# Kernel optimization log

Measured on AMD Instinct MI355X. Metric: run time of the kernel, lower is better.

The kernel has to match this reference:

```python
import jax, jax.numpy as jnp
import numpy as np

N_NODES = 50000
N_EDGES = 1600000
D = 64  # in_dim = hidden_dim = out_dim
R = 8   # num_rels


def setup_inputs() -> dict:
    key = jax.random.key(0)
    ks = jax.random.split(key, 9)
    adj = jax.random.randint(ks[0], (2, N_EDGES), 0, N_NODES, dtype=jnp.int32)
    features = jax.random.normal(ks[1], (N_NODES, D), dtype=jnp.float32)
    edge_type = jax.random.randint(ks[2], (N_EDGES,), 0, R, dtype=jnp.int32)
    s = 1.0 / np.sqrt(D)
    W1 = jax.random.normal(ks[3], (R, D, D), dtype=jnp.float32) * s
    root1 = jax.random.normal(ks[4], (D, D), dtype=jnp.float32) * s
    b1 = jnp.zeros((D,), dtype=jnp.float32)
    W2 = jax.random.normal(ks[5], (R, D, D), dtype=jnp.float32) * s
    root2 = jax.random.normal(ks[6], (D, D), dtype=jnp.float32) * s
    b2 = jnp.zeros((D,), dtype=jnp.float32)
    return {"adj": adj, "features": features, "edge_type": edge_type,
            "W1": W1, "root1": root1, "b1": b1,
            "W2": W2, "root2": root2, "b2": b2}


def _rgcn_layer(x, edge_index, edge_type, W, root, bias):
    # FastRGCNConv, aggr='add': out_i = sum_{(j,r)->i} W_r x_j + root^T x_i + b
    src, dst = edge_index[0], edge_index[1]
    # pre-transform all nodes under every relation: [R, N, F]
    h = jnp.einsum('nd,rdf->rnf', x, W)
    msg = h[edge_type, src]                      # [E, F] gather per edge
    agg = jax.ops.segment_sum(msg, dst, num_segments=x.shape[0])
    return agg + x @ root + bias


def reference(adj, features, edge_type, W1, root1, b1, W2, root2, b2):
    x = _rgcn_layer(features, adj, edge_type, W1, root1, b1)
    x = jax.nn.relu(x)
    x = _rgcn_layer(x, adj, edge_type, W2, root2, b2)
    return x
```

## Files before the change

### kernel.cpp

```cpp
#include <hip/hip_runtime.h>
#include <cstdint>
#include <cstddef>

#define DF 64
#define NREL 8
#define DPB 64
#define DPB_SHIFT 6
#define NBMAX 1024
#define EPB 4096
#define BCAP 3072
#define NKEY 512

typedef __attribute__((ext_vector_type(8))) short bf16x8;
typedef __attribute__((ext_vector_type(4))) float f32x4;

static __device__ __forceinline__ unsigned short f2bf(float f) {
  unsigned int u = __float_as_uint(f);
  u += 0x7FFFu + ((u >> 16) & 1u);
  return (unsigned short)(u >> 16);
}
static __device__ __forceinline__ float bf2f(unsigned short s) {
  return __uint_as_float((unsigned int)s << 16);
}

__global__ __launch_bounds__(256) void to_bf16(
    const float* __restrict__ x, unsigned short* __restrict__ xb, int n8)
{
  int i = blockIdx.x * 256 + threadIdx.x;
  if (i >= n8) return;
  const float4 v0 = *(const float4*)&x[(size_t)i * 8];
  const float4 v1 = *(const float4*)&x[(size_t)i * 8 + 4];
  uint4 pk;
  pk.x = (unsigned)f2bf(v0.x) | ((unsigned)f2bf(v0.y) << 16);
  pk.y = (unsigned)f2bf(v0.z) | ((unsigned)f2bf(v0.w) << 16);
  pk.z = (unsigned)f2bf(v1.x) | ((unsigned)f2bf(v1.y) << 16);
  pk.w = (unsigned)f2bf(v1.z) | ((unsigned)f2bf(v1.w) << 16);
  *(uint4*)&xb[(size_t)i * 8] = pk;
}

__global__ __launch_bounds__(512) void pack_wfrag(
    const float* __restrict__ W1, const float* __restrict__ rt1,
    const float* __restrict__ W2, const float* __restrict__ rt2,
    bf16x8* __restrict__ frag)
{
  const int mat = blockIdx.x;
  const float* W = (mat < 8)  ? (W1 + (size_t)mat * 4096)
                 : (mat == 8) ? rt1
                 : (mat < 17) ? (W2 + (size_t)(mat - 9) * 4096)
                              : rt2;
  const int idx = threadIdx.x;
  const int ft = idx >> 7;
  const int ks = (idx >> 6) & 1;
  const int l  = idx & 63;
  const int col = ft * 16 + (l & 15);
  const int k0  = ks * 32 + (l >> 4) * 8;
  bf16x8 f;
#pragma unroll
  for (int j = 0; j < 8; ++j)
    f[j] = (short)f2bf(W[(size_t)(k0 + j) * 64 + col]);
  frag[(((size_t)mat * 4 + ft) * 2 + ks) * 64 + l] = f;
}

__global__ __launch_bounds__(256) void zero_ints(int* __restrict__ p, int n)
{
  int i = blockIdx.x * 256 + threadIdx.x;
  if (i < n) p[i] = 0;
}

__global__ __launch_bounds__(512) void bucket_count(
    const int* __restrict__ dst, int* __restrict__ bcnt,
    int* __restrict__ relof, int E, int NB)
{
  __shared__ int lh[NBMAX];
  const int t = threadIdx.x;
  for (int i = t; i < NB; i += 512) lh[i] = 0;
  __syncthreads();
  const int base = blockIdx.x * EPB;
  const int cnt = min(EPB, E - base);
  for (int k = t; k < cnt; k += 512)
    atomicAdd(&lh[dst[base + k] >> DPB_SHIFT], 1);
  __syncthreads();
  int* rrow = relof + (size_t)blockIdx.x * NB;
  for (int i = t; i < NB; i += 512) {
    int c = lh[i];
    rrow[i] = c ? atomicAdd(&bcnt[i], c) : 0;
  }
}

__global__ __launch_bounds__(1024) void scan_buckets(
    const int* __restrict__ bcnt, int* __restrict__ boff, int NB, int E)
{
  __shared__ int sc[1024];
  const int t = threadIdx.x;
  int v = (t < NB) ? bcnt[t] : 0;
  sc[t] = v;
  __syncthreads();
  for (int off = 1; off < 1024; off <<= 1) {
    int u = (t >= off) ? sc[t - off] : 0;
    __syncthreads();
    sc[t] += u;
    __syncthreads();
  }
  if (t < NB) boff[t] = sc[t] - v;
  if (t == 0) boff[NB] = E;
}

__global__ __launch_bounds__(512) void bin_scatter(
    const int* __restrict__ src, const int* __restrict__ dst,
    const int* __restrict__ et,
    const int* __restrict__ boff, const int* __restrict__ relof,
    unsigned int* __restrict__ binned, int E, int NB)
{
  __shared__ int cur[NBMAX];
  const int t = threadIdx.x;
  const int* rrow = relof + (size_t)blockIdx.x * NB;
  for (int i = t; i < NB; i += 512) cur[i] = boff[i] + rrow[i];
  __syncthreads();
  const int base = blockIdx.x * EPB;
  const int cnt = min(EPB, E - base);
  for (int k = t; k < cnt; k += 512) {
    int e = base + k;
    int d = dst[e];
    int pos = atomicAdd(&cur[d >> DPB_SHIFT], 1);
    binned[pos] = ((unsigned)et[e] << 24) | ((unsigned)src[e] << 7) |
                  ((unsigned)d & (DPB - 1));
  }
}

static __device__ __forceinline__ void gadd(
    float* __restrict__ acc, const uint4& u)
{
  acc[0] += bf2f((unsigned short)u.x);
  acc[1] += bf2f((unsigned short)(u.x >> 16));
  acc[2] += bf2f((unsigned short)u.y);
  acc[3] += bf2f((unsigned short)(u.y >> 16));
  acc[4] += bf2f((unsigned short)u.z);
  acc[5] += bf2f((unsigned short)(u.z >> 16));
  acc[6] += bf2f((unsigned short)u.w);
  acc[7] += bf2f((unsigned short)(u.w >> 16));
}

__global__ __launch_bounds__(512) void gather_sum(
    const unsigned int* __restrict__ binned,
    const int* __restrict__ boff,
    const unsigned short* __restrict__ xb,
    unsigned short* __restrict__ s,
    int N)
{
  __shared__ unsigned int srt[BCAP];
  __shared__ int h[NKEY], sc[NKEY], cur[NKEY];
  const int t = threadIdx.x;
  const int b = blockIdx.x;
  const int beg = boff[b], end = boff[b + 1];
  const int m = min(end - beg, BCAP);

  h[t] = 0;
  __syncthreads();
  for (int k = t; k < m; k += 512) {
    unsigned w = binned[beg + k];
    atomicAdd(&h[((w & (DPB - 1)) << 3) | (w >> 24)], 1);
  }
  __syncthreads();
  sc[t] = h[t];
  __syncthreads();
  for (int off = 1; off < NKEY; off <<= 1) {
    int u = (t >= off) ? sc[t - off] : 0;
    __syncthreads();
    sc[t] += u;
    __syncthreads();
  }
  cur[t] = sc[t] - h[t];
  __syncthreads();
  for (int k = t; k < m; k += 512) {
    unsigned w = binned[beg + k];
    int pos = atomicAdd(&cur[((w & (DPB - 1)) << 3) | (w >> 24)], 1);
    srt[pos] = w;
  }
  __syncthreads();

  const int nl = t >> 3;
  const int node = (b << DPB_SHIFT) + nl;
  const int l8 = (t & 7) * 8;
  if (node >= N) return;
  const int ovf = end - beg - BCAP;

#define XADDR(wv) ((const uint4*)&xb[(((size_t)(((wv) >> 7) & 0x1FFFFu)) << 6) + l8])
  for (int r = 0; r < NREL; ++r) {
    const int kk = (nl << 3) | r;
    int p = sc[kk] - h[kk];
    const int pe = sc[kk];
    float acc[8];
#pragma unroll
    for (int i = 0; i < 8; ++i) acc[i] = 0.f;

    for (; p + 3 < pe; p += 4) {
      unsigned w0 = srt[p],     w1 = srt[p + 1];
      unsigned w2 = srt[p + 2], w3 = srt[p + 3];
      uint4 u0 = *XADDR(w0), u1 = *XADDR(w1);
      uint4 u2 = *XADDR(w2), u3 = *XADDR(w3);
      gadd(acc, u0); gadd(acc, u1); gadd(acc, u2); gadd(acc, u3);
    }
    for (; p < pe; ++p) {
      unsigned w0 = srt[p];
      uint4 u0 = *XADDR(w0);
      gadd(acc, u0);
    }
    if (ovf > 0) {
      for (int k = 0; k < ovf; ++k) {
        unsigned w0 = binned[beg + BCAP + k];
        if ((int)(w0 & (DPB - 1)) == nl && (int)(w0 >> 24) == r) {
          uint4 u0 = *XADDR(w0);
          gadd(acc, u0);
        }
      }
    }

    uint4 pk;
    pk.x = (unsigned)f2bf(acc[0]) | ((unsigned)f2bf(acc[1]) << 16);
    pk.y = (unsigned)f2bf(acc[2]) | ((unsigned)f2bf(acc[3]) << 16);
    pk.z = (unsigned)f2bf(acc[4]) | ((unsigned)f2bf(acc[5]) << 16);
    pk.w = (unsigned)f2bf(acc[6]) | ((unsigned)f2bf(acc[7]) << 16);
    *(uint4*)&s[(((size_t)node * NREL + r) << 6) + l8] = pk;
  }
#undef XADDR
}

__global__ __launch_bounds__(256) void gemm_fused(
    const unsigned short* __restrict__ s,
    const unsigned short* __restrict__ xb,
    const bf16x8* __restrict__ wfrag,
    const float* __restrict__ bias,
    float* __restrict__ out,
    unsigned short* __restrict__ xbn,
    int N, int do_relu)
{
  const int tid = threadIdx.x;
  const int l  = tid & 63;
  const int w  = tid >> 6;
  const int n0 = blockIdx.x * 128 + w * 32;
  const int lr = l & 15;
  const int lg = l >> 4;

  f32x4 acc[4][2];
#pragma unroll
  for (int mt = 0; mt < 4; ++mt)
#pragma unroll
    for (int nt = 0; nt < 2; ++nt)
      acc[mt][nt] = (f32x4)(0.f);

  const int node0 = n0 + lr;
  const int node1 = n0 + 16 + lr;

  for (int r = 0; r < 9; ++r) {
    const bf16x8* wf = wfrag + (size_t)r * 512;
    bf16x8 a[4][2];
#pragma unroll
    for (int mt = 0; mt < 4; ++mt)
#pragma unroll
      for (int ks = 0; ks < 2; ++ks)
        a[mt][ks] = wf[(mt * 2 + ks) * 64 + l];

    bf16x8 b[2][2];
#pragma unroll
    for (int nt = 0; nt < 2; ++nt) {
      const int node = nt ? node1 : node0;
#pragma unroll
      for (int ks = 0; ks < 2; ++ks) {
        if (node < N) {
          const unsigned short* bp = (r < 8)
              ? &s[(((size_t)node * NREL + r) << 6) + ks * 32 + lg * 8]
              : &xb[((size_t)node << 6) + ks * 32 + lg * 8];
          b[nt][ks] = *(const bf16x8*)bp;
        } else {
          b[nt][ks] = (bf16x8)(short)0;
        }
      }
    }

#pragma unroll
    for (int ks = 0; ks < 2; ++ks)
#pragma unroll
      for (int mt = 0; mt < 4; ++mt)
#pragma unroll
        for (int nt = 0; nt < 2; ++nt)
          acc[mt][nt] = __builtin_amdgcn_mfma_f32_16x16x32_bf16(
              a[mt][ks], b[nt][ks], acc[mt][nt], 0, 0, 0);
  }

#pragma unroll
  for (int nt = 0; nt < 2; ++nt) {
    const int node = nt ? node1 : node0;
    if (node < N) {
#pragma unroll
      for (int mt = 0; mt < 4; ++mt) {
        const int f0 = mt * 16 + lg * 4;
        float4 bb = *(const float4*)&bias[f0];
        float4 v = make_float4(acc[mt][nt][0] + bb.x,
                               acc[mt][nt][1] + bb.y,
                               acc[mt][nt][2] + bb.z,
                               acc[mt][nt][3] + bb.w);
        if (do_relu) {
          v.x = fmaxf(v.x, 0.f); v.y = fmaxf(v.y, 0.f);
          v.z = fmaxf(v.z, 0.f); v.w = fmaxf(v.w, 0.f);
        }
        *(float4*)&out[((size_t)node << 6) + f0] = v;
        if (xbn) {
          uint2 pk;
          pk.x = (unsigned)f2bf(v.x) | ((unsigned)f2bf(v.y) << 16);
          pk.y = (unsigned)f2bf(v.z) | ((unsigned)f2bf(v.w) << 16);
          *(uint2*)&xbn[((size_t)node << 6) + f0] = pk;
        }
      }
    }
  }
}

__global__ __launch_bounds__(128) void rgcn_transform(
    const float* __restrict__ x,
    const float* __restrict__ Wc,
    unsigned short* __restrict__ hb,
    int N)
{
  const int r = blockIdx.y;
  const float* W = Wc + (size_t)r * DF * DF;

  __shared__ float Ws[DF * DF];
  __shared__ float Xs[128 * 65];

  const int tid = threadIdx.x;
  const int n0 = blockIdx.x * 128;
  const int nrem = N - n0;

  {
    const float4* Wv = (const float4*)W;
    float4* Wsv = (float4*)Ws;
#pragma unroll
    for (int j = 0; j < 8; ++j) Wsv[tid + j * 128] = Wv[tid + j * 128];
  }
#pragma unroll
  for (int j = 0; j < 16; ++j) {
    int idx = tid + j * 128;
    int n = idx >> 4;
    int c4 = (idx & 15) * 4;
    float4 v = make_float4(0.f, 0.f, 0.f, 0.f);
    if (n < nrem) v = *(const float4*)&x[(size_t)(n0 + n) * DF + c4];
    float* p = &Xs[n * 65 + c4];
    p[0] = v.x; p[1] = v.y; p[2] = v.z; p[3] = v.w;
  }
  __syncthreads();

  const int fg = (tid & 7) * 8;
  const int ng = (tid >> 3) * 8;

  float4 a0[8], a1[8];
#pragma unroll
  for (int i = 0; i < 8; ++i) {
    a0[i] = make_float4(0.f, 0.f, 0.f, 0.f);
    a1[i] = make_float4(0.f, 0.f, 0.f, 0.f);
  }

#pragma unroll 4
  for (int d = 0; d < DF; ++d) {
    float4 w0 = *(const float4*)&Ws[d * DF + fg];
    float4 w1 = *(const float4*)&Ws[d * DF + fg + 4];
#pragma unroll
    for (int i = 0; i < 8; ++i) {
      float xv = Xs[(ng + i) * 65 + d];
      a0[i].x += xv * w0.x; a0[i].y += xv * w0.y;
      a0[i].z += xv * w0.z; a0[i].w += xv * w0.w;
      a1[i].x += xv * w1.x; a1[i].y += xv * w1.y;
      a1[i].z += xv * w1.z; a1[i].w += xv * w1.w;
    }
  }

#pragma unroll
  for (int i = 0; i < 8; ++i) {
    int n = ng + i;
    if (n < nrem) {
      uint4 pk;
      pk.x = (unsigned)f2bf(a0[i].x) | ((unsigned)f2bf(a0[i].y) << 16);
      pk.y = (unsigned)f2bf(a0[i].z) | ((unsigned)f2bf(a0[i].w) << 16);
      pk.z = (unsigned)f2bf(a1[i].x) | ((unsigned)f2bf(a1[i].y) << 16);
      pk.w = (unsigned)f2bf(a1[i].z) | ((unsigned)f2bf(a1[i].w) << 16);
      unsigned short* op = hb + (((size_t)r * N + (n0 + n)) << 6) + fg;
      *(uint4*)op = pk;
    }
  }
}

__global__ __launch_bounds__(128) void rgcn_root_epilogue(
    const float* __restrict__ x,
    const float* __restrict__ root,
    const float* __restrict__ bias,
    float* __restrict__ out,
    int N, int mode)
{
  __shared__ float Ws[DF * DF];
  __shared__ float Xs[128 * 65];

  const int tid = threadIdx.x;
  const int n0 = blockIdx.x * 128;
  const int nrem = N - n0;

  {
    const float4* Wv = (const float4*)root;
    float4* Wsv = (float4*)Ws;
#pragma unroll
    for (int j = 0; j < 8; ++j) Wsv[tid + j * 128] = Wv[tid + j * 128];
  }
#pragma unroll
  for (int j = 0; j < 16; ++j) {
    int idx = tid + j * 128;
    int n = idx >> 4;
    int c4 = (idx & 15) * 4;
    float4 v = make_float4(0.f, 0.f, 0.f, 0.f);
    if (n < nrem) v = *(const float4*)&x[(size_t)(n0 + n) * DF + c4];
    float* p = &Xs[n * 65 + c4];
    p[0] = v.x; p[1] = v.y; p[2] = v.z; p[3] = v.w;
  }
  __syncthreads();

  const int fg = (tid & 7) * 8;
  const int ng = (tid >> 3) * 8;

  float4 a0[8], a1[8];
#pragma unroll
  for (int i = 0; i < 8; ++i) {
    a0[i] = make_float4(0.f, 0.f, 0.f, 0.f);
    a1[i] = make_float4(0.f, 0.f, 0.f, 0.f);
  }

#pragma unroll 4
  for (int d = 0; d < DF; ++d) {
    float4 w0 = *(const float4*)&Ws[d * DF + fg];
    float4 w1 = *(const float4*)&Ws[d * DF + fg + 4];
#pragma unroll
    for (int i = 0; i < 8; ++i) {
      float xv = Xs[(ng + i) * 65 + d];
      a0[i].x += xv * w0.x; a0[i].y += xv * w0.y;
      a0[i].z += xv * w0.z; a0[i].w += xv * w0.w;
      a1[i].x += xv * w1.x; a1[i].y += xv * w1.y;
      a1[i].z += xv * w1.z; a1[i].w += xv * w1.w;
    }
  }

  float4 bb0 = *(const float4*)&bias[fg];
  float4 bb1 = *(const float4*)&bias[fg + 4];

#pragma unroll
  for (int i = 0; i < 8; ++i) {
    int n = ng + i;
    if (n < nrem) {
      float* op = out + (size_t)(n0 + n) * DF + fg;
      float4 o0 = *(float4*)op;
      float4 o1 = *(float4*)(op + 4);
      o0.x += a0[i].x + bb0.x; o0.y += a0[i].y + bb0.y;
      o0.z += a0[i].z + bb0.z; o0.w += a0[i].w + bb0.w;
      o1.x += a1[i].x + bb1.x; o1.y += a1[i].y + bb1.y;
      o1.z += a1[i].z + bb1.z; o1.w += a1[i].w + bb1.w;
      if (mode == 1) {
        o0.x = fmaxf(o0.x, 0.f); o0.y = fmaxf(o0.y, 0.f);
        o0.z = fmaxf(o0.z, 0.f); o0.w = fmaxf(o0.w, 0.f);
        o1.x = fmaxf(o1.x, 0.f); o1.y = fmaxf(o1.y, 0.f);
        o1.z = fmaxf(o1.z, 0.f); o1.w = fmaxf(o1.w, 0.f);
      }
      *(float4*)op = o0;
      *(float4*)(op + 4) = o1;
    }
  }
}

__global__ __launch_bounds__(256) void rgcn_scatter(
    const int* __restrict__ src, const int* __restrict__ dst,
    const int* __restrict__ et,
    const unsigned short* __restrict__ hb,
    float* __restrict__ out,
    int E, int N, int r0, int r1)
{
  long long g = (long long)blockIdx.x * 256 + threadIdx.x;
  int e = (int)(g >> 4);
  if (e >= E) return;
  int r = et[e];
  if (r < r0 || r >= r1) return;
  int f4 = ((int)g & 15) * 4;
  int s = src[e];
  int d = dst[e];
  ushort4 u = *(const ushort4*)&hb[(((size_t)(r - r0) * N + s) << 6) + f4];
  float* o = out + ((size_t)d << 6) + f4;
  atomicAdd(o + 0, bf2f(u.x));
  atomicAdd(o + 1, bf2f(u.y));
  atomicAdd(o + 2, bf2f(u.z));
  atomicAdd(o + 3, bf2f(u.w));
}

extern "C" void kernel_launch(void* const* d_in, const int* in_sizes, int n_in,
                              void* d_out, int out_size, void* d_ws, size_t ws_size,
                              hipStream_t stream) {
  const int* adj    = (const int*)d_in[0];
  const float* feat = (const float*)d_in[1];
  const int* et     = (const int*)d_in[2];
  const float* W1   = (const float*)d_in[3];
  const float* rt1  = (const float*)d_in[4];
  const float* b1   = (const float*)d_in[5];
  const float* W2   = (const float*)d_in[6];
  const float* rt2  = (const float*)d_in[7];
  const float* b2   = (const float*)d_in[8];

  const int E = in_sizes[0] / 2;
  const int N = in_sizes[1] / DF;
  const int* srcp = adj;
  const int* dstp = adj + E;

  float* out = (float*)d_out;
  const size_t ND = (size_t)N * DF;
  const int nblk = (N + 127) / 128;
  const int NB = (N + DPB - 1) >> DPB_SHIFT;
  const int ebk = (E + EPB - 1) / EPB;

  const size_t wfrag_elems = (size_t)18 * 512;
  const size_t need = 8 * ND * 2 + ND * 2 + ND * 2 + wfrag_elems * 16 +
                      (size_t)E * 4 + (size_t)ebk * NB * 4 +
                      ((size_t)2 * NB + 1) * 4;

  if (ws_size >= need && NB <= NBMAX && N < (1 << 17)) {
    unsigned short* s   = (unsigned short*)d_ws;
    unsigned short* xb  = s + 8 * ND;
    unsigned short* xb2 = xb + ND;
    bf16x8* wfrag = (bf16x8*)(xb2 + ND);
    unsigned int* binned = (unsigned int*)(wfrag + wfrag_elems);
    int* relof = (int*)(binned + E);
    int* bcnt = relof + (size_t)ebk * NB;
    int* boff = bcnt + NB;

    pack_wfrag<<<18, 512, 0, stream>>>(W1, rt1, W2, rt2, wfrag);
    to_bf16<<<(int)((ND / 8 + 255) / 256), 256, 0, stream>>>(feat, xb, (int)(ND / 8));

    zero_ints<<<(NB + 255) / 256, 256, 0, stream>>>(bcnt, NB);
    bucket_count<<<ebk, 512, 0, stream>>>(dstp, bcnt, relof, E, NB);
    scan_buckets<<<1, 1024, 0, stream>>>(bcnt, boff, NB, E);
    bin_scatter<<<ebk, 512, 0, stream>>>(srcp, dstp, et, boff, relof,
                                         binned, E, NB);

    gather_sum<<<NB, 512, 0, stream>>>(binned, boff, xb, s, N);
    gemm_fused<<<nblk, 256, 0, stream>>>(s, xb, wfrag, b1, out, xb2, N, 1);

    gather_sum<<<NB, 512, 0, stream>>>(binned, boff, xb2, s, N);
    gemm_fused<<<nblk, 256, 0, stream>>>(s, xb2, wfrag + (size_t)9 * 512,
                                         b2, out, nullptr, N, 0);
    return;
  }

  size_t per_rel = ND * sizeof(unsigned short);
  size_t xmid_b = ND * sizeof(float);
  int RC = 1;
  if (ws_size > per_rel + xmid_b) {
    size_t rc = (ws_size - xmid_b) / per_rel;
    RC = rc >= NREL ? NREL : (int)rc;
  }
  unsigned short* hb = (unsigned short*)d_ws;
  float* xmid = (float*)((char*)d_ws + (size_t)RC * per_rel);
  const int sblk = (int)(((size_t)E * 16 + 255) / 256);

  for (int layer = 0; layer < 2; ++layer) {
    const float* xin = layer ? xmid : feat;
    const float* W   = layer ? W2 : W1;
    const float* rt  = layer ? rt2 : rt1;
    const float* bs  = layer ? b2 : b1;
    float* o         = layer ? out : xmid;

    hipMemsetAsync(o, 0, ND * sizeof(float), stream);
    for (int r0 = 0; r0 < NREL; r0 += RC) {
      int rc = (NREL - r0) < RC ? (NREL - r0) : RC;
      rgcn_transform<<<dim3(nblk, rc), 128, 0, stream>>>(
          xin, W + (size_t)r0 * DF * DF, hb, N);
      rgcn_scatter<<<sblk, 256, 0, stream>>>(
          srcp, dstp, et, hb, o, E, N, r0, r0 + rc);
    }
    rgcn_root_epilogue<<<nblk, 128, 0, stream>>>(xin, rt, bs, o, N,
                                                 layer == 0 ? 1 : 2);
  }
}
```

Baseline: 155.7 us.

## Merge prep kernels, halve edges per binning block, use wave-shuffle scan

Three small preprocessing kernels (weight fragment packing, feature bf16 conversion, bucket counter zeroing) are merged into one launch to cut launch overhead. The edges-per-block constant for bucket counting and scatter is halved, giving more blocks for parallelism but a larger per-block offset table. The 512-entry prefix scan in gather_sum now uses wavefront shuffles plus a per-wave sum instead of a barrier-heavy Hillis-Steele loop.

```diff
diff --git a/kernel.cpp b/kernel.cpp
--- a/kernel.cpp
+++ b/kernel.cpp
@@ -7,7 +7,7 @@
 #define DPB 64
 #define DPB_SHIFT 6
 #define NBMAX 1024
-#define EPB 4096
+#define EPB 2048
 #define BCAP 3072
 #define NKEY 512
 
@@ -23,48 +23,49 @@
   return __uint_as_float((unsigned int)s << 16);
 }
 
-__global__ __launch_bounds__(256) void to_bf16(
-    const float* __restrict__ x, unsigned short* __restrict__ xb, int n8)
-{
-  int i = blockIdx.x * 256 + threadIdx.x;
-  if (i >= n8) return;
-  const float4 v0 = *(const float4*)&x[(size_t)i * 8];
-  const float4 v1 = *(const float4*)&x[(size_t)i * 8 + 4];
-  uint4 pk;
-  pk.x = (unsigned)f2bf(v0.x) | ((unsigned)f2bf(v0.y) << 16);
-  pk.y = (unsigned)f2bf(v0.z) | ((unsigned)f2bf(v0.w) << 16);
-  pk.z = (unsigned)f2bf(v1.x) | ((unsigned)f2bf(v1.y) << 16);
-  pk.w = (unsigned)f2bf(v1.z) | ((unsigned)f2bf(v1.w) << 16);
-  *(uint4*)&xb[(size_t)i * 8] = pk;
-}
-
-__global__ __launch_bounds__(512) void pack_wfrag(
+__global__ __launch_bounds__(512) void prep(
     const float* __restrict__ W1, const float* __restrict__ rt1,
     const float* __restrict__ W2, const float* __restrict__ rt2,
-    bf16x8* __restrict__ frag)
-{
-  const int mat = blockIdx.x;
-  const float* W = (mat < 8)  ? (W1 + (size_t)mat * 4096)
-                 : (mat == 8) ? rt1
-                 : (mat < 17) ? (W2 + (size_t)(mat - 9) * 4096)
+    bf16x8* __restrict__ frag,
+    const float* __restrict__ x, unsigned short* __restrict__ xb, int n8,
+    int* __restrict__ bcnt, int NB)
+{
+  const int b = blockIdx.x;
+  const int t = threadIdx.x;
+
+  if (b < 18) {
+    const float* W = (b < 8)  ? (W1 + (size_t)b * 4096)
+                   : (b == 8) ? rt1
+                   : (b < 17) ? (W2 + (size_t)(b - 9) * 4096)
                               : rt2;
-  const int idx = threadIdx.x;
-  const int ft = idx >> 7;
-  const int ks = (idx >> 6) & 1;
-  const int l  = idx & 63;
-  const int col = ft * 16 + (l & 15);
-  const int k0  = ks * 32 + (l >> 4) * 8;
-  bf16x8 f;
-#pragma unroll
-  for (int j = 0; j < 8; ++j)
-    f[j] = (short)f2bf(W[(size_t)(k0 + j) * 64 + col]);
-  frag[(((size_t)mat * 4 + ft) * 2 + ks) * 64 + l] = f;
-}
-
-__global__ __launch_bounds__(256) void zero_ints(int* __restrict__ p, int n)
-{
-  int i = blockIdx.x * 256 + threadIdx.x;
-  if (i < n) p[i] = 0;
+    const int ft = t >> 7;
+    const int ks = (t >> 6) & 1;
+    const int l  = t & 63;
+    const int col = ft * 16 + (l & 15);
+    const int k0  = ks * 32 + (l >> 4) * 8;
+    bf16x8 f;
+#pragma unroll
+    for (int j = 0; j < 8; ++j)
+      f[j] = (short)f2bf(W[(size_t)(k0 + j) * 64 + col]);
+    frag[(((size_t)b * 4 + ft) * 2 + ks) * 64 + l] = f;
+    return;
+  }
+
+  if (b == 18) {
+    for (int i = t; i < NB; i += 512) bcnt[i] = 0;
+  }
+
+  const int i = (b - 18) * 512 + t;
+  if (i < n8) {
+    const float4 v0 = *(const float4*)&x[(size_t)i * 8];
+    const float4 v1 = *(const float4*)&x[(size_t)i * 8 + 4];
+    uint4 pk;
+    pk.x = (unsigned)f2bf(v0.x) | ((unsigned)f2bf(v0.y) << 16);
+    pk.y = (unsigned)f2bf(v0.z) | ((unsigned)f2bf(v0.w) << 16);
+    pk.z = (unsigned)f2bf(v1.x) | ((unsigned)f2bf(v1.y) << 16);
+    pk.w = (unsigned)f2bf(v1.z) | ((unsigned)f2bf(v1.w) << 16);
+    *(uint4*)&xb[(size_t)i * 8] = pk;
+  }
 }
 
 __global__ __launch_bounds__(512) void bucket_count(
@@ -149,6 +150,7 @@
 {
   __shared__ unsigned int srt[BCAP];
   __shared__ int h[NKEY], sc[NKEY], cur[NKEY];
+  __shared__ int wsum[8];
   const int t = threadIdx.x;
   const int b = blockIdx.x;
   const int beg = boff[b], end = boff[b + 1];
@@ -161,16 +163,26 @@
     atomicAdd(&h[((w & (DPB - 1)) << 3) | (w >> 24)], 1);
   }
   __syncthreads();
-  sc[t] = h[t];
-  __syncthreads();
-  for (int off = 1; off < NKEY; off <<= 1) {
-    int u = (t >= off) ? sc[t - off] : 0;
+
+  {
+    const int lane = t & 63;
+    const int wv = t >> 6;
+    int v = h[t];
+    int incl = v;
+#pragma unroll
+    for (int off = 1; off < 64; off <<= 1) {
+      int u = __shfl_up(incl, off);
+      if (lane >= off) incl += u;
+    }
+    if (lane == 63) wsum[wv] = incl;
     __syncthreads();
-    sc[t] += u;
-    __syncthreads();
-  }
-  cur[t] = sc[t] - h[t];
-  __syncthreads();
+    int wo = 0;
+    for (int w2 = 0; w2 < wv; ++w2) wo += wsum[w2];
+    sc[t] = incl + wo;
+    cur[t] = sc[t] - v;
+  }
+  __syncthreads();
+
   for (int k = t; k < m; k += 512) {
     unsigned w = binned[beg + k];
     int pos = atomicAdd(&cur[((w & (DPB - 1)) << 3) | (w >> 24)], 1);
@@ -532,10 +544,10 @@
     int* bcnt = relof + (size_t)ebk * NB;
     int* boff = bcnt + NB;
 
-    pack_wfrag<<<18, 512, 0, stream>>>(W1, rt1, W2, rt2, wfrag);
-    to_bf16<<<(int)((ND / 8 + 255) / 256), 256, 0, stream>>>(feat, xb, (int)(ND / 8));
-
-    zero_ints<<<(NB + 255) / 256, 256, 0, stream>>>(bcnt, NB);
+    const int n8 = (int)(ND / 8);
+    prep<<<18 + (n8 + 511) / 512, 512, 0, stream>>>(
+        W1, rt1, W2, rt2, wfrag, feat, xb, n8, bcnt, NB);
+
     bucket_count<<<ebk, 512, 0, stream>>>(dstp, bcnt, relof, E, NB);
     scan_buckets<<<1, 1024, 0, stream>>>(bcnt, boff, NB, E);
     bin_scatter<<<ebk, 512, 0, stream>>>(srcp, dstp, et, boff, relof,
```

New measurement: 171.4 us. 10.1% more time.
